# Optimization experiments

Measured on AMD Instinct MI355X. Metric: run time of the kernel, lower is better.

## Reference

```python
import jax, jax.numpy as jnp
import numpy as np

B_G = 16        # number of point clouds
N_PER = 32768   # points per cloud (equal -> no padding)
T = B_G * N_PER
CIN = 16
D = 32          # global_dim
H = 4           # num_heads
HD = D // H
L = 2           # layers
EPS_LN = 1e-5
EPS_Z = 1e-6


def setup_inputs() -> dict:
    key = jax.random.key(0)
    ks = jax.random.split(key, 32)
    r = lambda i, shape, s: (jax.random.normal(ks[i], shape, dtype=jnp.float32) * s)
    inp = {
        "x": r(0, (T, CIN), 1.0),
        "pos": r(1, (T, 3), 1.0),
        "batch": (jnp.arange(T, dtype=jnp.int32) // N_PER),
        "w_in": r(2, (CIN, D), CIN ** -0.5),
        "b_in": r(3, (D,), 0.02),
        "w_pos": r(4, (3, D), 3 ** -0.5),
        "b_pos": r(5, (D,), 0.02),
        "wq": r(6, (L, D, D), D ** -0.5),
        "bq": r(7, (L, D), 0.02),
        "wk": r(8, (L, D, D), D ** -0.5),
        "bk": r(9, (L, D), 0.02),
        "wv": r(10, (L, D, D), D ** -0.5),
        "bv": r(11, (L, D), 0.02),
        "wo": r(12, (L, D, D), D ** -0.5),
        "bo": r(13, (L, D), 0.02),
        "g1": jnp.ones((L, D), jnp.float32),
        "be1": jnp.zeros((L, D), jnp.float32),
        "w1": r(14, (L, D, 2 * D), D ** -0.5),
        "bf1": r(15, (L, 2 * D), 0.02),
        "w2": r(16, (L, 2 * D, D), (2 * D) ** -0.5),
        "bf2": r(17, (L, D), 0.02),
        "g2": jnp.ones((L, D), jnp.float32),
        "be2": jnp.zeros((L, D), jnp.float32),
    }
    return inp


def _layernorm(h, g, b):
    mu = jnp.mean(h, axis=-1, keepdims=True)
    var = jnp.mean(jnp.square(h - mu), axis=-1, keepdims=True)
    return (h - mu) * jax.lax.rsqrt(var + EPS_LN) * g + b


def _linear_attn(h, wq, bq, wk, bk, wv, bv, wo, bo):
    B, N, C = h.shape
    def heads(w, b):
        return (h @ w + b).reshape(B, N, H, HD).transpose(0, 2, 1, 3)  # [B,H,N,hd]
    q = jax.nn.elu(heads(wq, bq)) + 1.0   # ELU feature map phi(.)
    k = jax.nn.elu(heads(wk, bk)) + 1.0
    v = heads(wv, bv)
    kv = jnp.einsum("bhnd,bhne->bhde", k, v)            # O(N) KV summary
    ksum = k.sum(axis=2)                                   # [B,H,hd]
    z = 1.0 / (jnp.einsum("bhnd,bhd->bhn", q, ksum) + EPS_Z)
    out = jnp.einsum("bhnd,bhde->bhne", q, kv) * z[..., None]
    out = out.transpose(0, 2, 1, 3).reshape(B, N, C)
    return out @ wo + bo


def reference(x, pos, batch, w_in, b_in, w_pos, b_pos, wq, bq, wk, bk, wv, bv,
              wo, bo, g1, be1, w1, bf1, w2, bf2, g2, be2):
    # to_dense_batch: batch is sorted; compute per-point index within its segment
    counts = jax.ops.segment_sum(jnp.ones((T,), jnp.int32), batch, num_segments=B_G)
    starts = jnp.concatenate([jnp.zeros((1,), jnp.int32), jnp.cumsum(counts)[:-1]])
    idx = jnp.arange(T, dtype=jnp.int32) - starts[batch]
    x_dense = jnp.zeros((B_G, N_PER, CIN), x.dtype).at[batch, idx].set(x)
    pos_dense = jnp.zeros((B_G, N_PER, 3), pos.dtype).at[batch, idx].set(pos)

    h = (x_dense @ w_in + b_in) + (pos_dense @ w_pos + b_pos)  # [B,N,D]
    for l in range(L):
        h = _layernorm(h + _linear_attn(h, wq[l], bq[l], wk[l], bk[l],
                                        wv[l], bv[l], wo[l], bo[l]), g1[l], be1[l])
        ffn = jax.nn.relu(h @ w1[l] + bf1[l]) @ w2[l] + bf2[l]
        h = _layernorm(h + ffn, g2[l], be2[l])
    return h[batch, idx]  # back to [T, D] (h[mask])
```

## Files before the change

### kernel.cpp

```cpp
#include <hip/hip_runtime.h>

#define KVSZ 288
#define EPS_LN 1e-5f
#define EPS_Z  1e-6f

typedef __attribute__((ext_vector_type(8))) short bf16x8;
typedef __attribute__((ext_vector_type(4))) float f32x4;

#define MFMA(a, b, c) __builtin_amdgcn_mfma_f32_16x16x32_bf16(a, b, c, 0, 0, 0)

#define PWE 0
#define LBASE(l) (1024 + (l) * 8192)
#define PQ 0
#define PO 1024
#define P1 2048
#define P2 4096
#define PK 6144
#define PV 7168

__device__ __forceinline__ unsigned short f2bf(float f) {
  union { float f; unsigned u; } x; x.f = f;
  unsigned r = x.u + 0x7fff + ((x.u >> 16) & 1);
  return (unsigned short)(r >> 16);
}

__device__ __forceinline__ unsigned pkbf(float a, float b) {
#if __has_builtin(__builtin_amdgcn_cvt_pk_bf16_f32)
  typedef __attribute__((ext_vector_type(2))) __bf16 bf16x2_t;
  bf16x2_t v = __builtin_amdgcn_cvt_pk_bf16_f32(a, b);
  return __builtin_bit_cast(unsigned, v);
#else
  return (unsigned)f2bf(a) | ((unsigned)f2bf(b) << 16);
#endif
}

__device__ __forceinline__ float bfu(unsigned short s) {
  union { float f; unsigned u; } x; x.u = ((unsigned)s) << 16; return x.f;
}

__device__ __forceinline__ void lds_fence() { asm volatile("s_waitcnt lgkmcnt(0)" ::: "memory"); }
__device__ __forceinline__ float phi(float x) { return x > 0.f ? x + 1.f : __expf(x); }

__device__ __forceinline__ int perm32(int kp) {
  return ((kp & 4) << 2) | (((kp >> 3) << 2) + (kp & 3));
}

__device__ __forceinline__ bf16x8 bbuild(f32x4 lo, f32x4 hi) {
  union { bf16x8 v; unsigned u[4]; } cv;
  cv.u[0] = pkbf(lo[0], lo[1]); cv.u[1] = pkbf(lo[2], lo[3]);
  cv.u[2] = pkbf(hi[0], hi[1]); cv.u[3] = pkbf(hi[2], hi[3]);
  return cv.v;
}

__device__ __forceinline__ void stage_a32(unsigned short* dst, const float* __restrict__ W,
                                          int N, int gt, int gs) {
  for (int i = gt; i < 32 * N; i += gs) {
    int n = i >> 5, kp = i & 31;
    dst[i] = f2bf(W[perm32(kp) * N + n]);
  }
}
__device__ __forceinline__ void stage_a64(unsigned short* dst, const float* __restrict__ W,
                                          int gt, int gs) {
  for (int i = gt; i < 64 * 32; i += gs) {
    int n = i >> 6, kp = i & 63;
    int kl = ((kp >> 5) << 5) + perm32(kp & 31);
    dst[i] = f2bf(W[kl * 32 + n]);
  }
}

__device__ __forceinline__ void stage_kvm_lds(unsigned short* dst,
                                              const float* __restrict__ kvg, int tid) {
  for (int i = tid; i < 1024; i += 256) {
    int e = i >> 5, kp = i & 31;
    int d = perm32(kp);
    float v = ((d >> 3) == (e >> 3)) ? kvg[(e >> 3) * 64 + (d & 7) * 8 + (e & 7)] : 0.f;
    dst[i] = f2bf(v);
  }
}

__device__ __forceinline__ void ln_t(f32x4& a0, f32x4& a1, float4 g0, float4 g1,
                                     float4 b0, float4 b1) {
  float s = a0[0] + a0[1] + a0[2] + a0[3] + a1[0] + a1[1] + a1[2] + a1[3];
  s += __shfl_xor(s, 16); s += __shfl_xor(s, 32);
  float mu = s * (1.f / 32.f);
  float vv = 0.f;
#pragma unroll
  for (int r = 0; r < 4; r++) {
    a0[r] -= mu; a1[r] -= mu;
    vv += a0[r] * a0[r] + a1[r] * a1[r];
  }
  vv += __shfl_xor(vv, 16); vv += __shfl_xor(vv, 32);
  float rstd = rsqrtf(vv * (1.f / 32.f) + EPS_LN);
  a0[0] = a0[0] * rstd * g0.x + b0.x; a0[1] = a0[1] * rstd * g0.y + b0.y;
  a0[2] = a0[2] * rstd * g0.z + b0.z; a0[3] = a0[3] * rstd * g0.w + b0.w;
  a1[0] = a1[0] * rstd * g1.x + b1.x; a1[1] = a1[1] * rstd * g1.y + b1.y;
  a1[2] = a1[2] * rstd * g1.z + b1.z; a1[3] = a1[3] * rstd * g1.w + b1.w;
}

__device__ __forceinline__ void layer_core_l(
    f32x4 (&hc0)[4], f32x4 (&hc1)[4], const bf16x8 (&hBp)[4],
    const unsigned short* lw, const unsigned short* kvm, const float* kss,
    int quad, int m,
    const float* __restrict__ bq, const float* __restrict__ bo,
    const float* __restrict__ g1, const float* __restrict__ be1,
    const float* __restrict__ bf1, const float* __restrict__ bf2,
    const float* __restrict__ g2, const float* __restrict__ be2) {
  const int k0 = quad * 8, q4 = quad * 4;
  {
    const bf16x8 wqA0 = *(const bf16x8*)(lw + PQ + m * 32 + k0);
    const bf16x8 wqA1 = *(const bf16x8*)(lw + PQ + (16 + m) * 32 + k0);
    const bf16x8 woA0 = *(const bf16x8*)(lw + PO + m * 32 + k0);
    const bf16x8 woA1 = *(const bf16x8*)(lw + PO + (16 + m) * 32 + k0);
    const bf16x8 kvA0 = *(const bf16x8*)(kvm + m * 32 + k0);
    const bf16x8 kvA1 = *(const bf16x8*)(kvm + (16 + m) * 32 + k0);
    const float4 bq0 = *(const float4*)(bq + q4), bq1 = *(const float4*)(bq + 16 + q4);
    const float4 bo0 = *(const float4*)(bo + q4), bo1 = *(const float4*)(bo + 16 + q4);
    const float4 g10 = *(const float4*)(g1 + q4), g11 = *(const float4*)(g1 + 16 + q4);
    const float4 e10 = *(const float4*)(be1 + q4), e11 = *(const float4*)(be1 + 16 + q4);
    const float4 ks0 = *(const float4*)(kss + q4);
    const float4 ks1 = *(const float4*)(kss + 16 + q4);
#pragma unroll
    for (int mt = 0; mt < 4; mt++) {
      f32x4 q0 = {bq0.x, bq0.y, bq0.z, bq0.w};
      f32x4 q1 = {bq1.x, bq1.y, bq1.z, bq1.w};
      q0 = MFMA(wqA0, hBp[mt], q0);
      q1 = MFMA(wqA1, hBp[mt], q1);
#pragma unroll
      for (int r = 0; r < 4; r++) { q0[r] = phi(q0[r]); q1[r] = phi(q1[r]); }
      bf16x8 qB = bbuild(q0, q1);
      f32x4 zz = {0.f, 0.f, 0.f, 0.f};
      f32x4 at0 = MFMA(kvA0, qB, zz);
      f32x4 at1 = MFMA(kvA1, qB, zz);
      float p0 = q0[0] * ks0.x + q0[1] * ks0.y + q0[2] * ks0.z + q0[3] * ks0.w;
      float p1 = q1[0] * ks1.x + q1[1] * ks1.y + q1[2] * ks1.z + q1[3] * ks1.w;
      p0 += __shfl_xor(p0, 16);
      p1 += __shfl_xor(p1, 16);
      float z0 = 1.f / (p0 + EPS_Z), z1 = 1.f / (p1 + EPS_Z);
      bf16x8 aB;
      {
        union { bf16x8 v; unsigned u[4]; } cv;
        cv.u[0] = pkbf(at0[0] * z0, at0[1] * z0); cv.u[1] = pkbf(at0[2] * z0, at0[3] * z0);
        cv.u[2] = pkbf(at1[0] * z1, at1[1] * z1); cv.u[3] = pkbf(at1[2] * z1, at1[3] * z1);
        aB = cv.v;
      }
      f32x4 h0 = hc0[mt], h1 = hc1[mt];
      h0[0] += bo0.x; h0[1] += bo0.y; h0[2] += bo0.z; h0[3] += bo0.w;
      h1[0] += bo1.x; h1[1] += bo1.y; h1[2] += bo1.z; h1[3] += bo1.w;
      h0 = MFMA(woA0, aB, h0);
      h1 = MFMA(woA1, aB, h1);
      ln_t(h0, h1, g10, g11, e10, e11);
      hc0[mt] = h0; hc1[mt] = h1;
    }
  }
  {
    bf16x8 w1A[4]; float4 b1f[4];
#pragma unroll
    for (int nt = 0; nt < 4; nt++) {
      w1A[nt] = *(const bf16x8*)(lw + P1 + (nt * 16 + m) * 32 + k0);
      b1f[nt] = *(const float4*)(bf1 + nt * 16 + q4);
    }
    const bf16x8 w2L0 = *(const bf16x8*)(lw + P2 + m * 64 + k0);
    const bf16x8 w2H0 = *(const bf16x8*)(lw + P2 + m * 64 + 32 + k0);
    const bf16x8 w2L1 = *(const bf16x8*)(lw + P2 + (16 + m) * 64 + k0);
    const bf16x8 w2H1 = *(const bf16x8*)(lw + P2 + (16 + m) * 64 + 32 + k0);
    const float4 b20 = *(const float4*)(bf2 + q4), b21 = *(const float4*)(bf2 + 16 + q4);
    const float4 g20 = *(const float4*)(g2 + q4), g21 = *(const float4*)(g2 + 16 + q4);
    const float4 e20 = *(const float4*)(be2 + q4), e21 = *(const float4*)(be2 + 16 + q4);
#pragma unroll
    for (int mt = 0; mt < 4; mt++) {
      bf16x8 hB = bbuild(hc0[mt], hc1[mt]);
      f32x4 hd[4];
#pragma unroll
      for (int nt = 0; nt < 4; nt++) {
        f32x4 ini = {b1f[nt].x, b1f[nt].y, b1f[nt].z, b1f[nt].w};
        hd[nt] = MFMA(w1A[nt], hB, ini);
#pragma unroll
        for (int r = 0; r < 4; r++) hd[nt][r] = fmaxf(hd[nt][r], 0.f);
      }
      bf16x8 fL = bbuild(hd[0], hd[1]);
      bf16x8 fH = bbuild(hd[2], hd[3]);
      f32x4 o0 = hc0[mt], o1 = hc1[mt];
      o0[0] += b20.x; o0[1] += b20.y; o0[2] += b20.z; o0[3] += b20.w;
      o1[0] += b21.x; o1[1] += b21.y; o1[2] += b21.z; o1[3] += b21.w;
      o0 = MFMA(w2L0, fL, o0);
      o0 = MFMA(w2H0, fH, o0);
      o1 = MFMA(w2L1, fL, o1);
      o1 = MFMA(w2H1, fH, o1);
      ln_t(o0, o1, g20, g21, e20, e21);
      hc0[mt] = o0; hc1[mt] = o1;
    }
  }
}

__device__ __forceinline__ void kv_stage_l(
    const bf16x8 (&hBp)[4], unsigned short* tw,
    const unsigned short* lwK, const unsigned short* lwV,
    float* blk, int quad, int m,
    const float* __restrict__ bk, const float* __restrict__ bv) {
  const int k0 = quad * 8, q4 = quad * 4;
  unsigned short* Tk = tw;
  unsigned short* Tv = tw + 1280;
  const bf16x8 wkA0 = *(const bf16x8*)(lwK + m * 32 + k0);
  const bf16x8 wkA1 = *(const bf16x8*)(lwK + (16 + m) * 32 + k0);
  const bf16x8 wvA0 = *(const bf16x8*)(lwV + m * 32 + k0);
  const bf16x8 wvA1 = *(const bf16x8*)(lwV + (16 + m) * 32 + k0);
  const float4 bk0 = *(const float4*)(bk + q4), bk1 = *(const float4*)(bk + 16 + q4);
  const float4 bv0 = *(const float4*)(bv + q4), bv1 = *(const float4*)(bv + 16 + q4);
  f32x4 accA = {0.f, 0.f, 0.f, 0.f}, accB = {0.f, 0.f, 0.f, 0.f};
  f32x4 ksa0 = {0.f, 0.f, 0.f, 0.f}, ksa1 = {0.f, 0.f, 0.f, 0.f};
#pragma unroll
  for (int ch = 0; ch < 2; ch++) {
#pragma unroll
    for (int mtl = 0; mtl < 2; mtl++) {
      int mt = ch * 2 + mtl;
      f32x4 kn0 = {bk0.x, bk0.y, bk0.z, bk0.w};
      f32x4 kn1 = {bk1.x, bk1.y, bk1.z, bk1.w};
      f32x4 vn0 = {bv0.x, bv0.y, bv0.z, bv0.w};
      f32x4 vn1 = {bv1.x, bv1.y, bv1.z, bv1.w};
      kn0 = MFMA(wkA0, hBp[mt], kn0);
      kn1 = MFMA(wkA1, hBp[mt], kn1);
      vn0 = MFMA(wvA0, hBp[mt], vn0);
      vn1 = MFMA(wvA1, hBp[mt], vn1);
      int cb = mtl * 16 + m;
#pragma unroll
      for (int r = 0; r < 4; r++) {
        kn0[r] = phi(kn0[r]); kn1[r] = phi(kn1[r]);
        ksa0[r] += kn0[r];    ksa1[r] += kn1[r];
        Tk[(q4 + r) * 40 + cb]      = f2bf(kn0[r]);
        Tk[(16 + q4 + r) * 40 + cb] = f2bf(kn1[r]);
        Tv[(q4 + r) * 40 + cb]      = f2bf(vn0[r]);
        Tv[(16 + q4 + r) * 40 + cb] = f2bf(vn1[r]);
      }
    }
    lds_fence();
    bf16x8 akL = *(const bf16x8*)(Tk + m * 40 + k0);
    bf16x8 akH = *(const bf16x8*)(Tk + (16 + m) * 40 + k0);
    bf16x8 avL = *(const bf16x8*)(Tv + m * 40 + k0);
    bf16x8 avH = *(const bf16x8*)(Tv + (16 + m) * 40 + k0);
    accA = MFMA(akL, avL, accA);
    accB = MFMA(akH, avH, accB);
    lds_fence();
  }
#pragma unroll
  for (int r = 0; r < 4; r++) {
    float v0 = ksa0[r], v1 = ksa1[r];
    v0 += __shfl_xor(v0, 1); v0 += __shfl_xor(v0, 2); v0 += __shfl_xor(v0, 4); v0 += __shfl_xor(v0, 8);
    v1 += __shfl_xor(v1, 1); v1 += __shfl_xor(v1, 2); v1 += __shfl_xor(v1, 4); v1 += __shfl_xor(v1, 8);
    if (m == 0) {
      atomicAdd(&blk[256 + q4 + r], v0);
      atomicAdd(&blk[272 + q4 + r], v1);
    }
  }
  if ((quad >> 1) == (m >> 3)) {
    int h0 = quad >> 1, h1 = 2 + (quad >> 1), e = m & 7;
#pragma unroll
    for (int r = 0; r < 4; r++) {
      int d = (q4 + r) & 7;
      atomicAdd(&blk[h0 * 64 + d * 8 + e], accA[r]);
      atomicAdd(&blk[h1 * 64 + d * 8 + e], accB[r]);
    }
  }
}

__global__ __launch_bounds__(256) void k_prep(
    const float* __restrict__ w_in, const float* __restrict__ w_pos,
    const float* __restrict__ wq, const float* __restrict__ wk,
    const float* __restrict__ wv, const float* __restrict__ wo,
    const float* __restrict__ w1, const float* __restrict__ w2,
    unsigned short* __restrict__ pw, float* __restrict__ kvbuf) {
  const int gt = blockIdx.x * 256 + threadIdx.x;
  const int gs = gridDim.x * 256;
  for (int i = gt; i < 2 * 16 * KVSZ; i += gs) kvbuf[i] = 0.f;
  for (int i = gt; i < 1024; i += gs) {
    int n = i >> 5, k = i & 31;
    float v = k < 16 ? w_in[k * 32 + n] : (k < 19 ? w_pos[(k - 16) * 32 + n] : 0.f);
    pw[PWE + i] = f2bf(v);
  }
  for (int l = 0; l < 2; l++) {
    unsigned short* b = pw + LBASE(l);
    stage_a32(b + PQ, wq + l * 1024, 32, gt, gs);
    stage_a32(b + PO, wo + l * 1024, 32, gt, gs);
    stage_a32(b + P1, w1 + l * 2048, 64, gt, gs);
    stage_a64(b + P2, w2 + l * 2048, gt, gs);
    stage_a32(b + PK, wk + l * 1024, 32, gt, gs);
    stage_a32(b + PV, wv + l * 1024, 32, gt, gs);
  }
}

template <int H16>
__global__ __launch_bounds__(256) void k_embed(
    const float* __restrict__ x, const float* __restrict__ pos,
    const float* __restrict__ b_in, const float* __restrict__ b_pos,
    const float* __restrict__ bk, const float* __restrict__ bv,
    const unsigned short* __restrict__ pw, unsigned short* __restrict__ hb,
    float* __restrict__ hf, float* __restrict__ gkv) {
  __shared__ __align__(16) unsigned short lws[3072];
  __shared__ __align__(16) unsigned short tiles[4 * 2560];
  __shared__ float blk[KVSZ];
  const int tid = threadIdx.x;
  const int wv_ = tid >> 6, lane = tid & 63, quad = lane >> 4, m = lane & 15;
  unsigned short* tw = tiles + wv_ * 2560;
  const int cloud = blockIdx.x >> 7;
  const int wbase = blockIdx.x * 256 + wv_ * 64;
  const int k0 = quad * 8, q4 = quad * 4;
  float4 xt0[4], xt1[4];
  float pp0[4], pp1[4], pp2[4];
#pragma unroll
  for (int mt = 0; mt < 4; mt++) {
    int p = wbase + mt * 16 + m;
    if (quad < 2) {
      const float4* xp = (const float4*)(x + (size_t)p * 16 + quad * 8);
      xt0[mt] = xp[0]; xt1[mt] = xp[1];
    } else if (quad == 2) {
      const float* pq = pos + (size_t)p * 3;
      pp0[mt] = pq[0]; pp1[mt] = pq[1]; pp2[mt] = pq[2];
    }
  }
  for (int j = tid; j < 384; j += 256) {
    int i = j * 8;
    const unsigned short* src = (i < 1024) ? (pw + PWE + i)
                                           : (pw + LBASE(0) + PK + (i - 1024));
    *(bf16x8*)(lws + i) = *(const bf16x8*)src;
  }
  for (int i = tid; i < KVSZ; i += 256) blk[i] = 0.f;
  __syncthreads();
  const bf16x8 weA0 = *(const bf16x8*)(lws + m * 32 + k0);
  const bf16x8 weA1 = *(const bf16x8*)(lws + (16 + m) * 32 + k0);
  float4 bi0, bi1;
  {
    float4 a = *(const float4*)(b_in + q4), b = *(const float4*)(b_pos + q4);
    bi0 = make_float4(a.x + b.x, a.y + b.y, a.z + b.z, a.w + b.w);
    float4 c = *(const float4*)(b_in + 16 + q4), d = *(const float4*)(b_pos + 16 + q4);
    bi1 = make_float4(c.x + d.x, c.y + d.y, c.z + d.z, c.w + d.w);
  }
  bf16x8 fr[4];
#pragma unroll
  for (int mt = 0; mt < 4; mt++) {
    int p = wbase + mt * 16 + m;
    union { bf16x8 v; unsigned u[4]; } xb;
    xb.u[0] = xb.u[1] = xb.u[2] = xb.u[3] = 0;
    if (quad < 2) {
      xb.u[0] = pkbf(xt0[mt].x, xt0[mt].y); xb.u[1] = pkbf(xt0[mt].z, xt0[mt].w);
      xb.u[2] = pkbf(xt1[mt].x, xt1[mt].y); xb.u[3] = pkbf(xt1[mt].z, xt1[mt].w);
    } else if (quad == 2) {
      xb.u[0] = pkbf(pp0[mt], pp1[mt]); xb.u[1] = pkbf(pp2[mt], 0.f);
    }
    f32x4 i0 = {bi0.x, bi0.y, bi0.z, bi0.w};
    f32x4 i1 = {bi1.x, bi1.y, bi1.z, bi1.w};
    f32x4 h0 = MFMA(weA0, xb.v, i0);
    f32x4 h1 = MFMA(weA1, xb.v, i1);
    fr[mt] = bbuild(h0, h1);
    if (H16) {
      *(bf16x8*)(hb + ((size_t)p * 32 + quad * 8)) = fr[mt];
    } else {
      float* hp = hf + (size_t)p * 32;
      *(float4*)(hp + q4)      = make_float4(h0[0], h0[1], h0[2], h0[3]);
      *(float4*)(hp + 16 + q4) = make_float4(h1[0], h1[1], h1[2], h1[3]);
    }
  }
  kv_stage_l(fr, tw, lws + 1024, lws + 2048, blk, quad, m, bk, bv);
  __syncthreads();
  float* g = gkv + cloud * KVSZ;
  for (int i = tid; i < KVSZ; i += 256) atomicAdd(&g[i], blk[i]);
}

template <int H16>
__global__ __launch_bounds__(256) void k_mid(
    const float* __restrict__ bq, const float* __restrict__ bo,
    const float* __restrict__ g1, const float* __restrict__ be1,
    const float* __restrict__ bf1, const float* __restrict__ bf2,
    const float* __restrict__ g2, const float* __restrict__ be2,
    const float* __restrict__ bkn, const float* __restrict__ bvn,
    const unsigned short* __restrict__ pw, const float* __restrict__ kv_in,
    float* __restrict__ gkv_out, unsigned short* __restrict__ hb,
    float* __restrict__ hf) {
  __shared__ __align__(16) unsigned short lws[8192];
  __shared__ __align__(16) unsigned short kvm[1024];
  __shared__ __align__(16) float kss[32];
  __shared__ __align__(16) unsigned short tiles[4 * 2560];
  __shared__ float blk[KVSZ];
  const int tid = threadIdx.x;
  const int wv_ = tid >> 6, lane = tid & 63, quad = lane >> 4, m = lane & 15;
  unsigned short* tw = tiles + wv_ * 2560;
  const int cloud = blockIdx.x >> 7;
  const int wbase = blockIdx.x * 256 + wv_ * 64;
  const int q4 = quad * 4;
  const float* kvg = kv_in + cloud * KVSZ;
  bf16x8 fr[4];
  if (H16) {
#pragma unroll
    for (int mt = 0; mt < 4; mt++) {
      int p = wbase + mt * 16 + m;
      fr[mt] = *(const bf16x8*)(hb + ((size_t)p * 32 + quad * 8));
    }
  }
  for (int j = tid; j < 1024; j += 256) {
    int i = j * 8;
    const unsigned short* src = (i < 6144) ? (pw + LBASE(0) + i)
                                           : (pw + LBASE(1) + PK + (i - 6144));
    *(bf16x8*)(lws + i) = *(const bf16x8*)src;
  }
  stage_kvm_lds(kvm, kvg, tid);
  if (tid < 32) kss[tid] = kvg[256 + tid];
  for (int i = tid; i < KVSZ; i += 256) blk[i] = 0.f;
  __syncthreads();
  f32x4 hc0[4], hc1[4];
#pragma unroll
  for (int mt = 0; mt < 4; mt++) {
    if (H16) {
#pragma unroll
      for (int r = 0; r < 4; r++) {
        hc0[mt][r] = bfu((unsigned short)fr[mt][r]);
        hc1[mt][r] = bfu((unsigned short)fr[mt][4 + r]);
      }
    } else {
      int p = wbase + mt * 16 + m;
      const float* hp = hf + (size_t)p * 32;
      float4 lo = *(const float4*)(hp + q4);
      float4 hi = *(const float4*)(hp + 16 + q4);
      hc0[mt][0] = lo.x; hc0[mt][1] = lo.y; hc0[mt][2] = lo.z; hc0[mt][3] = lo.w;
      hc1[mt][0] = hi.x; hc1[mt][1] = hi.y; hc1[mt][2] = hi.z; hc1[mt][3] = hi.w;
      fr[mt] = bbuild(hc0[mt], hc1[mt]);
    }
  }
  layer_core_l(hc0, hc1, fr, lws, kvm, kss, quad, m,
               bq, bo, g1, be1, bf1, bf2, g2, be2);
#pragma unroll
  for (int mt = 0; mt < 4; mt++) {
    int p = wbase + mt * 16 + m;
    fr[mt] = bbuild(hc0[mt], hc1[mt]);
    if (H16) {
      *(bf16x8*)(hb + ((size_t)p * 32 + quad * 8)) = fr[mt];
    } else {
      float* hp = hf + (size_t)p * 32;
      *(float4*)(hp + q4)      = make_float4(hc0[mt][0], hc0[mt][1], hc0[mt][2], hc0[mt][3]);
      *(float4*)(hp + 16 + q4) = make_float4(hc1[mt][0], hc1[mt][1], hc1[mt][2], hc1[mt][3]);
    }
  }
  kv_stage_l(fr, tw, lws + 6144, lws + 7168, blk, quad, m, bkn, bvn);
  __syncthreads();
  float* g = gkv_out + cloud * KVSZ;
  for (int i = tid; i < KVSZ; i += 256) atomicAdd(&g[i], blk[i]);
}

template <int H16>
__global__ __launch_bounds__(256) void k_last(
    const float* __restrict__ bq, const float* __restrict__ bo,
    const float* __restrict__ g1, const float* __restrict__ be1,
    const float* __restrict__ bf1, const float* __restrict__ bf2,
    const float* __restrict__ g2, const float* __restrict__ be2,
    const unsigned short* __restrict__ pw, const float* __restrict__ kv_in,
    const unsigned short* __restrict__ hb, float* __restrict__ out) {
  __shared__ __align__(16) unsigned short lws[6144];
  __shared__ __align__(16) unsigned short kvm[1024];
  __shared__ __align__(16) float kss[32];
  const int tid = threadIdx.x;
  const int wv_ = tid >> 6, lane = tid & 63, quad = lane >> 4, m = lane & 15;
  const int cloud = blockIdx.x >> 7;
  const int wbase = blockIdx.x * 256 + wv_ * 64;
  const int q4 = quad * 4;
  const float* kvg = kv_in + cloud * KVSZ;
  bf16x8 fr[4];
  if (H16) {
#pragma unroll
    for (int mt = 0; mt < 4; mt++) {
      int p = wbase + mt * 16 + m;
      fr[mt] = *(const bf16x8*)(hb + ((size_t)p * 32 + quad * 8));
    }
  }
  for (int j = tid; j < 768; j += 256)
    *(bf16x8*)(lws + j * 8) = *(const bf16x8*)(pw + LBASE(1) + j * 8);
  stage_kvm_lds(kvm, kvg, tid);
  if (tid < 32) kss[tid] = kvg[256 + tid];
  __syncthreads();
  f32x4 hc0[4], hc1[4];
#pragma unroll
  for (int mt = 0; mt < 4; mt++) {
    if (H16) {
#pragma unroll
      for (int r = 0; r < 4; r++) {
        hc0[mt][r] = bfu((unsigned short)fr[mt][r]);
        hc1[mt][r] = bfu((unsigned short)fr[mt][4 + r]);
      }
    } else {
      int p = wbase + mt * 16 + m;
      const float* hp = out + (size_t)p * 32;
      float4 lo = *(const float4*)(hp + q4);
      float4 hi = *(const float4*)(hp + 16 + q4);
      hc0[mt][0] = lo.x; hc0[mt][1] = lo.y; hc0[mt][2] = lo.z; hc0[mt][3] = lo.w;
      hc1[mt][0] = hi.x; hc1[mt][1] = hi.y; hc1[mt][2] = hi.z; hc1[mt][3] = hi.w;
      fr[mt] = bbuild(hc0[mt], hc1[mt]);
    }
  }
  layer_core_l(hc0, hc1, fr, lws, kvm, kss, quad, m,
               bq, bo, g1, be1, bf1, bf2, g2, be2);
#pragma unroll
  for (int mt = 0; mt < 4; mt++) {
    int p = wbase + mt * 16 + m;
    float* hp = out + (size_t)p * 32;
    *(float4*)(hp + q4)      = make_float4(hc0[mt][0], hc0[mt][1], hc0[mt][2], hc0[mt][3]);
    *(float4*)(hp + 16 + q4) = make_float4(hc1[mt][0], hc1[mt][1], hc1[mt][2], hc1[mt][3]);
  }
}

extern "C" void kernel_launch(void* const* d_in, const int* in_sizes, int n_in,
                              void* d_out, int out_size, void* d_ws, size_t ws_size,
                              hipStream_t stream) {
  (void)in_sizes; (void)n_in; (void)out_size;
  const float* x     = (const float*)d_in[0];
  const float* pos   = (const float*)d_in[1];
  const float* w_in  = (const float*)d_in[3];
  const float* b_in  = (const float*)d_in[4];
  const float* w_pos = (const float*)d_in[5];
  const float* b_pos = (const float*)d_in[6];
  const float* wq  = (const float*)d_in[7];
  const float* bq  = (const float*)d_in[8];
  const float* wk  = (const float*)d_in[9];
  const float* bk  = (const float*)d_in[10];
  const float* wv  = (const float*)d_in[11];
  const float* bv  = (const float*)d_in[12];
  const float* wo  = (const float*)d_in[13];
  const float* bo  = (const float*)d_in[14];
  const float* g1  = (const float*)d_in[15];
  const float* be1 = (const float*)d_in[16];
  const float* w1  = (const float*)d_in[17];
  const float* bf1 = (const float*)d_in[18];
  const float* w2  = (const float*)d_in[19];
  const float* bf2 = (const float*)d_in[20];
  const float* g2  = (const float*)d_in[21];
  const float* be2 = (const float*)d_in[22];
  float* out = (float*)d_out;
  float* kvbuf = (float*)d_ws;
  unsigned short* pw = (unsigned short*)((char*)d_ws + 40960);
  unsigned short* hb = (unsigned short*)((char*)d_ws + 131072);
  const size_t need = 131072ull + 524288ull * 32ull * 2ull;
  const bool h16 = ws_size >= need;

  k_prep<<<dim3(64), dim3(256), 0, stream>>>(w_in, w_pos, wq, wk, wv, wo, w1, w2,
                                             pw, kvbuf);
  dim3 grid(2048), block(256);
  if (h16) {
    k_embed<1><<<grid, block, 0, stream>>>(x, pos, b_in, b_pos, bk, bv, pw, hb, out, kvbuf);
    k_mid<1><<<grid, block, 0, stream>>>(bq, bo, g1, be1, bf1, bf2, g2, be2,
                                         bk + 32, bv + 32, pw, kvbuf,
                                         kvbuf + 16 * KVSZ, hb, out);
    k_last<1><<<grid, block, 0, stream>>>(bq + 32, bo + 32, g1 + 32, be1 + 32,
                                          bf1 + 64, bf2 + 32, g2 + 32, be2 + 32,
                                          pw, kvbuf + 16 * KVSZ, hb, out);
  } else {
    k_embed<0><<<grid, block, 0, stream>>>(x, pos, b_in, b_pos, bk, bv, pw, hb, out, kvbuf);
    k_mid<0><<<grid, block, 0, stream>>>(bq, bo, g1, be1, bf1, bf2, g2, be2,
                                         bk + 32, bv + 32, pw, kvbuf,
                                         kvbuf + 16 * KVSZ, hb, out);
    k_last<0><<<grid, block, 0, stream>>>(bq + 32, bo + 32, g1 + 32, be1 + 32,
                                          bf1 + 64, bf2 + 32, g2 + 32, be2 + 32,
                                          pw, kvbuf + 16 * KVSZ, hb, out);
  }
}
```

Baseline: 250.4 us.

## Fuse embed/mid/last kernels into one persistent kernel with grid barriers

Replaces the three per-stage launches (embed, mid, last) with one persistent kernel of 512 blocks. Each block handles four 256-point chunks and uses atomic-counter grid barriers between the KV-summary phases. Global KV sums are read back via atomic RMW, so the reads see other blocks' accumulations. This removes two kernel launches and the drain/refill gaps between them, and reuses LDS-staged weights across chunks. In exchange it relies on all 512 blocks being co-resident and risks spin-wait cost and lower parallelism; it also packs K/V bf16 conversions pairwise.

```diff
diff --git a/kernel.cpp b/kernel.cpp
--- a/kernel.cpp
+++ b/kernel.cpp
@@ -3,6 +3,7 @@
 #define KVSZ 288
 #define EPS_LN 1e-5f
 #define EPS_Z  1e-6f
+#define NBLK 512
 
 typedef __attribute__((ext_vector_type(8))) short bf16x8;
 typedef __attribute__((ext_vector_type(4))) float f32x4;
@@ -41,6 +42,24 @@
 __device__ __forceinline__ void lds_fence() { asm volatile("s_waitcnt lgkmcnt(0)" ::: "memory"); }
 __device__ __forceinline__ float phi(float x) { return x > 0.f ? x + 1.f : __expf(x); }
 
+__device__ __forceinline__ float gread_rmw(const float* p) {
+  return atomicAdd((float*)p, 0.0f);
+}
+
+__device__ __forceinline__ void grid_barrier(unsigned* ctr) {
+  __syncthreads();
+  if (threadIdx.x == 0) {
+    __threadfence();
+    atomicAdd(ctr, 1u);
+    while (atomicAdd(ctr, 0u) < NBLK) __builtin_amdgcn_s_sleep(2);
+  }
+  __syncthreads();
+}
+
+__device__ __forceinline__ int swz_bid() {
+  return (blockIdx.x & 7) * (NBLK >> 3) + (blockIdx.x >> 3);
+}
+
 __device__ __forceinline__ int perm32(int kp) {
   return ((kp & 4) << 2) | (((kp >> 3) << 2) + (kp & 3));
 }
@@ -68,12 +87,12 @@
   }
 }
 
-__device__ __forceinline__ void stage_kvm_lds(unsigned short* dst,
+__device__ __forceinline__ void stage_kvm_rmw(unsigned short* dst,
                                               const float* __restrict__ kvg, int tid) {
   for (int i = tid; i < 1024; i += 256) {
     int e = i >> 5, kp = i & 31;
     int d = perm32(kp);
-    float v = ((d >> 3) == (e >> 3)) ? kvg[(e >> 3) * 64 + (d & 7) * 8 + (e & 7)] : 0.f;
+    float v = ((d >> 3) == (e >> 3)) ? gread_rmw(&kvg[(e >> 3) * 64 + (d & 7) * 8 + (e & 7)]) : 0.f;
     dst[i] = f2bf(v);
   }
 }
@@ -226,10 +245,12 @@
       for (int r = 0; r < 4; r++) {
         kn0[r] = phi(kn0[r]); kn1[r] = phi(kn1[r]);
         ksa0[r] += kn0[r];    ksa1[r] += kn1[r];
-        Tk[(q4 + r) * 40 + cb]      = f2bf(kn0[r]);
-        Tk[(16 + q4 + r) * 40 + cb] = f2bf(kn1[r]);
-        Tv[(q4 + r) * 40 + cb]      = f2bf(vn0[r]);
-        Tv[(16 + q4 + r) * 40 + cb] = f2bf(vn1[r]);
+        unsigned kk = pkbf(kn0[r], kn1[r]);
+        unsigned vv = pkbf(vn0[r], vn1[r]);
+        Tk[(q4 + r) * 40 + cb]      = (unsigned short)kk;
+        Tk[(16 + q4 + r) * 40 + cb] = (unsigned short)(kk >> 16);
+        Tv[(q4 + r) * 40 + cb]      = (unsigned short)vv;
+        Tv[(16 + q4 + r) * 40 + cb] = (unsigned short)(vv >> 16);
       }
     }
     lds_fence();
@@ -270,7 +291,7 @@
     unsigned short* __restrict__ pw, float* __restrict__ kvbuf) {
   const int gt = blockIdx.x * 256 + threadIdx.x;
   const int gs = gridDim.x * 256;
-  for (int i = gt; i < 2 * 16 * KVSZ; i += gs) kvbuf[i] = 0.f;
+  for (int i = gt; i < 2 * 16 * KVSZ + 16; i += gs) kvbuf[i] = 0.f;
   for (int i = gt; i < 1024; i += gs) {
     int n = i >> 5, k = i & 31;
     float v = k < 16 ? w_in[k * 32 + n] : (k < 19 ? w_pos[(k - 16) * 32 + n] : 0.f);
@@ -288,92 +309,16 @@
 }
 
 template <int H16>
-__global__ __launch_bounds__(256) void k_embed(
+__global__ __launch_bounds__(256, 2) void k_main(
     const float* __restrict__ x, const float* __restrict__ pos,
     const float* __restrict__ b_in, const float* __restrict__ b_pos,
-    const float* __restrict__ bk, const float* __restrict__ bv,
-    const unsigned short* __restrict__ pw, unsigned short* __restrict__ hb,
-    float* __restrict__ hf, float* __restrict__ gkv) {
-  __shared__ __align__(16) unsigned short lws[3072];
-  __shared__ __align__(16) unsigned short tiles[4 * 2560];
-  __shared__ float blk[KVSZ];
-  const int tid = threadIdx.x;
-  const int wv_ = tid >> 6, lane = tid & 63, quad = lane >> 4, m = lane & 15;
-  unsigned short* tw = tiles + wv_ * 2560;
-  const int cloud = blockIdx.x >> 7;
-  const int wbase = blockIdx.x * 256 + wv_ * 64;
-  const int k0 = quad * 8, q4 = quad * 4;
-  float4 xt0[4], xt1[4];
-  float pp0[4], pp1[4], pp2[4];
-#pragma unroll
-  for (int mt = 0; mt < 4; mt++) {
-    int p = wbase + mt * 16 + m;
-    if (quad < 2) {
-      const float4* xp = (const float4*)(x + (size_t)p * 16 + quad * 8);
-      xt0[mt] = xp[0]; xt1[mt] = xp[1];
-    } else if (quad == 2) {
-      const float* pq = pos + (size_t)p * 3;
-      pp0[mt] = pq[0]; pp1[mt] = pq[1]; pp2[mt] = pq[2];
-    }
-  }
-  for (int j = tid; j < 384; j += 256) {
-    int i = j * 8;
-    const unsigned short* src = (i < 1024) ? (pw + PWE + i)
-                                           : (pw + LBASE(0) + PK + (i - 1024));
-    *(bf16x8*)(lws + i) = *(const bf16x8*)src;
-  }
-  for (int i = tid; i < KVSZ; i += 256) blk[i] = 0.f;
-  __syncthreads();
-  const bf16x8 weA0 = *(const bf16x8*)(lws + m * 32 + k0);
-  const bf16x8 weA1 = *(const bf16x8*)(lws + (16 + m) * 32 + k0);
-  float4 bi0, bi1;
-  {
-    float4 a = *(const float4*)(b_in + q4), b = *(const float4*)(b_pos + q4);
-    bi0 = make_float4(a.x + b.x, a.y + b.y, a.z + b.z, a.w + b.w);
-    float4 c = *(const float4*)(b_in + 16 + q4), d = *(const float4*)(b_pos + 16 + q4);
-    bi1 = make_float4(c.x + d.x, c.y + d.y, c.z + d.z, c.w + d.w);
-  }
-  bf16x8 fr[4];
-#pragma unroll
-  for (int mt = 0; mt < 4; mt++) {
-    int p = wbase + mt * 16 + m;
-    union { bf16x8 v; unsigned u[4]; } xb;
-    xb.u[0] = xb.u[1] = xb.u[2] = xb.u[3] = 0;
-    if (quad < 2) {
-      xb.u[0] = pkbf(xt0[mt].x, xt0[mt].y); xb.u[1] = pkbf(xt0[mt].z, xt0[mt].w);
-      xb.u[2] = pkbf(xt1[mt].x, xt1[mt].y); xb.u[3] = pkbf(xt1[mt].z, xt1[mt].w);
-    } else if (quad == 2) {
-      xb.u[0] = pkbf(pp0[mt], pp1[mt]); xb.u[1] = pkbf(pp2[mt], 0.f);
-    }
-    f32x4 i0 = {bi0.x, bi0.y, bi0.z, bi0.w};
-    f32x4 i1 = {bi1.x, bi1.y, bi1.z, bi1.w};
-    f32x4 h0 = MFMA(weA0, xb.v, i0);
-    f32x4 h1 = MFMA(weA1, xb.v, i1);
-    fr[mt] = bbuild(h0, h1);
-    if (H16) {
-      *(bf16x8*)(hb + ((size_t)p * 32 + quad * 8)) = fr[mt];
-    } else {
-      float* hp = hf + (size_t)p * 32;
-      *(float4*)(hp + q4)      = make_float4(h0[0], h0[1], h0[2], h0[3]);
-      *(float4*)(hp + 16 + q4) = make_float4(h1[0], h1[1], h1[2], h1[3]);
-    }
-  }
-  kv_stage_l(fr, tw, lws + 1024, lws + 2048, blk, quad, m, bk, bv);
-  __syncthreads();
-  float* g = gkv + cloud * KVSZ;
-  for (int i = tid; i < KVSZ; i += 256) atomicAdd(&g[i], blk[i]);
-}
-
-template <int H16>
-__global__ __launch_bounds__(256) void k_mid(
-    const float* __restrict__ bq, const float* __restrict__ bo,
+    const float* __restrict__ bq, const float* __restrict__ bk,
+    const float* __restrict__ bv, const float* __restrict__ bo,
     const float* __restrict__ g1, const float* __restrict__ be1,
     const float* __restrict__ bf1, const float* __restrict__ bf2,
     const float* __restrict__ g2, const float* __restrict__ be2,
-    const float* __restrict__ bkn, const float* __restrict__ bvn,
-    const unsigned short* __restrict__ pw, const float* __restrict__ kv_in,
-    float* __restrict__ gkv_out, unsigned short* __restrict__ hb,
-    float* __restrict__ hf) {
+    const unsigned short* __restrict__ pw, float* __restrict__ kvbuf,
+    unsigned short* __restrict__ hb, float* __restrict__ out) {
   __shared__ __align__(16) unsigned short lws[8192];
   __shared__ __align__(16) unsigned short kvm[1024];
   __shared__ __align__(16) float kss[32];
@@ -382,124 +327,161 @@
   const int tid = threadIdx.x;
   const int wv_ = tid >> 6, lane = tid & 63, quad = lane >> 4, m = lane & 15;
   unsigned short* tw = tiles + wv_ * 2560;
-  const int cloud = blockIdx.x >> 7;
-  const int wbase = blockIdx.x * 256 + wv_ * 64;
-  const int q4 = quad * 4;
-  const float* kvg = kv_in + cloud * KVSZ;
-  bf16x8 fr[4];
-  if (H16) {
+  const int bid = swz_bid();
+  const int cloud = bid >> 5;
+  float* gkv0 = kvbuf + cloud * KVSZ;
+  float* gkv1 = kvbuf + (16 + cloud) * KVSZ;
+  unsigned* ctrs = (unsigned*)(kvbuf + 2 * 16 * KVSZ);
+  const int k0 = quad * 8, q4 = quad * 4;
+
+  for (int j = tid; j < 384; j += 256) {
+    int i = j * 8;
+    const unsigned short* src = (i < 1024) ? (pw + PWE + i)
+                                           : (pw + LBASE(0) + PK + (i - 1024));
+    *(bf16x8*)(lws + i) = *(const bf16x8*)src;
+  }
+  float4 bi0, bi1;
+  {
+    float4 a = *(const float4*)(b_in + q4), b = *(const float4*)(b_pos + q4);
+    bi0 = make_float4(a.x + b.x, a.y + b.y, a.z + b.z, a.w + b.w);
+    float4 c = *(const float4*)(b_in + 16 + q4), d = *(const float4*)(b_pos + 16 + q4);
+    bi1 = make_float4(c.x + d.x, c.y + d.y, c.z + d.z, c.w + d.w);
+  }
+  __syncthreads();
+  for (int c = 0; c < 4; c++) {
+    const int wbase = (bid * 4 + c) * 256 + wv_ * 64;
+    for (int i = tid; i < KVSZ; i += 256) blk[i] = 0.f;
+    __syncthreads();
+    const bf16x8 weA0 = *(const bf16x8*)(lws + m * 32 + k0);
+    const bf16x8 weA1 = *(const bf16x8*)(lws + (16 + m) * 32 + k0);
+    bf16x8 fr[4];
 #pragma unroll
     for (int mt = 0; mt < 4; mt++) {
       int p = wbase + mt * 16 + m;
-      fr[mt] = *(const bf16x8*)(hb + ((size_t)p * 32 + quad * 8));
-    }
-  }
+      union { bf16x8 v; unsigned u[4]; } xb;
+      xb.u[0] = xb.u[1] = xb.u[2] = xb.u[3] = 0;
+      if (quad < 2) {
+        const float4* xp = (const float4*)(x + (size_t)p * 16 + quad * 8);
+        float4 t0 = xp[0], t1 = xp[1];
+        xb.u[0] = pkbf(t0.x, t0.y); xb.u[1] = pkbf(t0.z, t0.w);
+        xb.u[2] = pkbf(t1.x, t1.y); xb.u[3] = pkbf(t1.z, t1.w);
+      } else if (quad == 2) {
+        const float* pp = pos + (size_t)p * 3;
+        xb.u[0] = pkbf(pp[0], pp[1]); xb.u[1] = pkbf(pp[2], 0.f);
+      }
+      f32x4 i0 = {bi0.x, bi0.y, bi0.z, bi0.w};
+      f32x4 i1 = {bi1.x, bi1.y, bi1.z, bi1.w};
+      f32x4 h0 = MFMA(weA0, xb.v, i0);
+      f32x4 h1 = MFMA(weA1, xb.v, i1);
+      fr[mt] = bbuild(h0, h1);
+      if (H16) {
+        *(bf16x8*)(hb + ((size_t)p * 32 + quad * 8)) = fr[mt];
+      } else {
+        float* hp = out + (size_t)p * 32;
+        *(float4*)(hp + q4)      = make_float4(h0[0], h0[1], h0[2], h0[3]);
+        *(float4*)(hp + 16 + q4) = make_float4(h1[0], h1[1], h1[2], h1[3]);
+      }
+    }
+    kv_stage_l(fr, tw, lws + 1024, lws + 2048, blk, quad, m, bk, bv);
+    __syncthreads();
+    for (int i = tid; i < KVSZ; i += 256) atomicAdd(&gkv0[i], blk[i]);
+    __syncthreads();
+  }
+  grid_barrier(&ctrs[0]);
+
   for (int j = tid; j < 1024; j += 256) {
     int i = j * 8;
     const unsigned short* src = (i < 6144) ? (pw + LBASE(0) + i)
                                            : (pw + LBASE(1) + PK + (i - 6144));
     *(bf16x8*)(lws + i) = *(const bf16x8*)src;
   }
-  stage_kvm_lds(kvm, kvg, tid);
-  if (tid < 32) kss[tid] = kvg[256 + tid];
-  for (int i = tid; i < KVSZ; i += 256) blk[i] = 0.f;
+  stage_kvm_rmw(kvm, gkv0, tid);
+  if (tid < 32) kss[tid] = gread_rmw(gkv0 + 256 + tid);
   __syncthreads();
-  f32x4 hc0[4], hc1[4];
-#pragma unroll
-  for (int mt = 0; mt < 4; mt++) {
-    if (H16) {
-#pragma unroll
-      for (int r = 0; r < 4; r++) {
-        hc0[mt][r] = bfu((unsigned short)fr[mt][r]);
-        hc1[mt][r] = bfu((unsigned short)fr[mt][4 + r]);
-      }
-    } else {
+  for (int c = 0; c < 4; c++) {
+    const int wbase = (bid * 4 + c) * 256 + wv_ * 64;
+    for (int i = tid; i < KVSZ; i += 256) blk[i] = 0.f;
+    __syncthreads();
+    f32x4 hc0[4], hc1[4];
+    bf16x8 fr[4];
+#pragma unroll
+    for (int mt = 0; mt < 4; mt++) {
       int p = wbase + mt * 16 + m;
-      const float* hp = hf + (size_t)p * 32;
-      float4 lo = *(const float4*)(hp + q4);
-      float4 hi = *(const float4*)(hp + 16 + q4);
-      hc0[mt][0] = lo.x; hc0[mt][1] = lo.y; hc0[mt][2] = lo.z; hc0[mt][3] = lo.w;
-      hc1[mt][0] = hi.x; hc1[mt][1] = hi.y; hc1[mt][2] = hi.z; hc1[mt][3] = hi.w;
+      if (H16) {
+        fr[mt] = *(const bf16x8*)(hb + ((size_t)p * 32 + quad * 8));
+#pragma unroll
+        for (int r = 0; r < 4; r++) {
+          hc0[mt][r] = bfu((unsigned short)fr[mt][r]);
+          hc1[mt][r] = bfu((unsigned short)fr[mt][4 + r]);
+        }
+      } else {
+        const float* hp = out + (size_t)p * 32;
+        float4 lo = *(const float4*)(hp + q4);
+        float4 hi = *(const float4*)(hp + 16 + q4);
+        hc0[mt][0] = lo.x; hc0[mt][1] = lo.y; hc0[mt][2] = lo.z; hc0[mt][3] = lo.w;
+        hc1[mt][0] = hi.x; hc1[mt][1] = hi.y; hc1[mt][2] = hi.z; hc1[mt][3] = hi.w;
+        fr[mt] = bbuild(hc0[mt], hc1[mt]);
+      }
+    }
+    layer_core_l(hc0, hc1, fr, lws, kvm, kss, quad, m,
+                 bq, bo, g1, be1, bf1, bf2, g2, be2);
+#pragma unroll
+    for (int mt = 0; mt < 4; mt++) {
+      int p = wbase + mt * 16 + m;
       fr[mt] = bbuild(hc0[mt], hc1[mt]);
-    }
-  }
-  layer_core_l(hc0, hc1, fr, lws, kvm, kss, quad, m,
-               bq, bo, g1, be1, bf1, bf2, g2, be2);
-#pragma unroll
-  for (int mt = 0; mt < 4; mt++) {
-    int p = wbase + mt * 16 + m;
-    fr[mt] = bbuild(hc0[mt], hc1[mt]);
-    if (H16) {
-      *(bf16x8*)(hb + ((size_t)p * 32 + quad * 8)) = fr[mt];
-    } else {
-      float* hp = hf + (size_t)p * 32;
+      if (H16) {
+        *(bf16x8*)(hb + ((size_t)p * 32 + quad * 8)) = fr[mt];
+      } else {
+        float* hp = out + (size_t)p * 32;
+        *(float4*)(hp + q4)      = make_float4(hc0[mt][0], hc0[mt][1], hc0[mt][2], hc0[mt][3]);
+        *(float4*)(hp + 16 + q4) = make_float4(hc1[mt][0], hc1[mt][1], hc1[mt][2], hc1[mt][3]);
+      }
+    }
+    kv_stage_l(fr, tw, lws + 6144, lws + 7168, blk, quad, m, bk + 32, bv + 32);
+    __syncthreads();
+    for (int i = tid; i < KVSZ; i += 256) atomicAdd(&gkv1[i], blk[i]);
+    __syncthreads();
+  }
+  grid_barrier(&ctrs[1]);
+
+  for (int j = tid; j < 768; j += 256)
+    *(bf16x8*)(lws + j * 8) = *(const bf16x8*)(pw + LBASE(1) + j * 8);
+  stage_kvm_rmw(kvm, gkv1, tid);
+  if (tid < 32) kss[tid] = gread_rmw(gkv1 + 256 + tid);
+  __syncthreads();
+  for (int c = 0; c < 4; c++) {
+    const int wbase = (bid * 4 + c) * 256 + wv_ * 64;
+    f32x4 hc0[4], hc1[4];
+    bf16x8 fr[4];
+#pragma unroll
+    for (int mt = 0; mt < 4; mt++) {
+      int p = wbase + mt * 16 + m;
+      if (H16) {
+        fr[mt] = *(const bf16x8*)(hb + ((size_t)p * 32 + quad * 8));
+#pragma unroll
+        for (int r = 0; r < 4; r++) {
+          hc0[mt][r] = bfu((unsigned short)fr[mt][r]);
+          hc1[mt][r] = bfu((unsigned short)fr[mt][4 + r]);
+        }
+      } else {
+        const float* hp = out + (size_t)p * 32;
+        float4 lo = *(const float4*)(hp + q4);
+        float4 hi = *(const float4*)(hp + 16 + q4);
+        hc0[mt][0] = lo.x; hc0[mt][1] = lo.y; hc0[mt][2] = lo.z; hc0[mt][3] = lo.w;
+        hc1[mt][0] = hi.x; hc1[mt][1] = hi.y; hc1[mt][2] = hi.z; hc1[mt][3] = hi.w;
+        fr[mt] = bbuild(hc0[mt], hc1[mt]);
+      }
+    }
+    layer_core_l(hc0, hc1, fr, lws, kvm, kss, quad, m,
+                 bq + 32, bo + 32, g1 + 32, be1 + 32, bf1 + 64, bf2 + 32,
+                 g2 + 32, be2 + 32);
+#pragma unroll
+    for (int mt = 0; mt < 4; mt++) {
+      int p = wbase + mt * 16 + m;
+      float* hp = out + (size_t)p * 32;
       *(float4*)(hp + q4)      = make_float4(hc0[mt][0], hc0[mt][1], hc0[mt][2], hc0[mt][3]);
       *(float4*)(hp + 16 + q4) = make_float4(hc1[mt][0], hc1[mt][1], hc1[mt][2], hc1[mt][3]);
     }
-  }
-  kv_stage_l(fr, tw, lws + 6144, lws + 7168, blk, quad, m, bkn, bvn);
-  __syncthreads();
-  float* g = gkv_out + cloud * KVSZ;
-  for (int i = tid; i < KVSZ; i += 256) atomicAdd(&g[i], blk[i]);
-}
-
-template <int H16>
-__global__ __launch_bounds__(256) void k_last(
-    const float* __restrict__ bq, const float* __restrict__ bo,
-    const float* __restrict__ g1, const float* __restrict__ be1,
-    const float* __restrict__ bf1, const float* __restrict__ bf2,
-    const float* __restrict__ g2, const float* __restrict__ be2,
-    const unsigned short* __restrict__ pw, const float* __restrict__ kv_in,
-    const unsigned short* __restrict__ hb, float* __restrict__ out) {
-  __shared__ __align__(16) unsigned short lws[6144];
-  __shared__ __align__(16) unsigned short kvm[1024];
-  __shared__ __align__(16) float kss[32];
-  const int tid = threadIdx.x;
-  const int wv_ = tid >> 6, lane = tid & 63, quad = lane >> 4, m = lane & 15;
-  const int cloud = blockIdx.x >> 7;
-  const int wbase = blockIdx.x * 256 + wv_ * 64;
-  const int q4 = quad * 4;
-  const float* kvg = kv_in + cloud * KVSZ;
-  bf16x8 fr[4];
-  if (H16) {
-#pragma unroll
-    for (int mt = 0; mt < 4; mt++) {
-      int p = wbase + mt * 16 + m;
-      fr[mt] = *(const bf16x8*)(hb + ((size_t)p * 32 + quad * 8));
-    }
-  }
-  for (int j = tid; j < 768; j += 256)
-    *(bf16x8*)(lws + j * 8) = *(const bf16x8*)(pw + LBASE(1) + j * 8);
-  stage_kvm_lds(kvm, kvg, tid);
-  if (tid < 32) kss[tid] = kvg[256 + tid];
-  __syncthreads();
-  f32x4 hc0[4], hc1[4];
-#pragma unroll
-  for (int mt = 0; mt < 4; mt++) {
-    if (H16) {
-#pragma unroll
-      for (int r = 0; r < 4; r++) {
-        hc0[mt][r] = bfu((unsigned short)fr[mt][r]);
-        hc1[mt][r] = bfu((unsigned short)fr[mt][4 + r]);
-      }
-    } else {
-      int p = wbase + mt * 16 + m;
-      const float* hp = out + (size_t)p * 32;
-      float4 lo = *(const float4*)(hp + q4);
-      float4 hi = *(const float4*)(hp + 16 + q4);
-      hc0[mt][0] = lo.x; hc0[mt][1] = lo.y; hc0[mt][2] = lo.z; hc0[mt][3] = lo.w;
-      hc1[mt][0] = hi.x; hc1[mt][1] = hi.y; hc1[mt][2] = hi.z; hc1[mt][3] = hi.w;
-      fr[mt] = bbuild(hc0[mt], hc1[mt]);
-    }
-  }
-  layer_core_l(hc0, hc1, fr, lws, kvm, kss, quad, m,
-               bq, bo, g1, be1, bf1, bf2, g2, be2);
-#pragma unroll
-  for (int mt = 0; mt < 4; mt++) {
-    int p = wbase + mt * 16 + m;
-    float* hp = out + (size_t)p * 32;
-    *(float4*)(hp + q4)      = make_float4(hc0[mt][0], hc0[mt][1], hc0[mt][2], hc0[mt][3]);
-    *(float4*)(hp + 16 + q4) = make_float4(hc1[mt][0], hc1[mt][1], hc1[mt][2], hc1[mt][3]);
   }
 }
 
@@ -538,22 +520,13 @@
 
   k_prep<<<dim3(64), dim3(256), 0, stream>>>(w_in, w_pos, wq, wk, wv, wo, w1, w2,
                                              pw, kvbuf);
-  dim3 grid(2048), block(256);
   if (h16) {
-    k_embed<1><<<grid, block, 0, stream>>>(x, pos, b_in, b_pos, bk, bv, pw, hb, out, kvbuf);
-    k_mid<1><<<grid, block, 0, stream>>>(bq, bo, g1, be1, bf1, bf2, g2, be2,
-                                         bk + 32, bv + 32, pw, kvbuf,
-                                         kvbuf + 16 * KVSZ, hb, out);
-    k_last<1><<<grid, block, 0, stream>>>(bq + 32, bo + 32, g1 + 32, be1 + 32,
-                                          bf1 + 64, bf2 + 32, g2 + 32, be2 + 32,
-                                          pw, kvbuf + 16 * KVSZ, hb, out);
+    k_main<1><<<dim3(NBLK), dim3(256), 0, stream>>>(
+        x, pos, b_in, b_pos, bq, bk, bv, bo, g1, be1, bf1, bf2, g2, be2,
+        pw, kvbuf, hb, out);
   } else {
-    k_embed<0><<<grid, block, 0, stream>>>(x, pos, b_in, b_pos, bk, bv, pw, hb, out, kvbuf);
-    k_mid<0><<<grid, block, 0, stream>>>(bq, bo, g1, be1, bf1, bf2, g2, be2,
-                                         bk + 32, bv + 32, pw, kvbuf,
-                                         kvbuf + 16 * KVSZ, hb, out);
-    k_last<0><<<grid, block, 0, stream>>>(bq + 32, bo + 32, g1 + 32, be1 + 32,
-                                          bf1 + 64, bf2 + 32, g2 + 32, be2 + 32,
-                                          pw, kvbuf + 16 * KVSZ, hb, out);
-  }
-}
+    k_main<0><<<dim3(NBLK), dim3(256), 0, stream>>>(
+        x, pos, b_in, b_pos, bq, bk, bv, bo, g1, be1, bf1, bf2, g2, be2,
+        pw, kvbuf, hb, out);
+  }
+}
```

After: 346.4 us. 38.4% more time.
